# Performance work log

Hardware: AMD Instinct MI355X
Metric: run time of the kernel (lower is better)

Reference implementation:

```python
import jax, jax.numpy as jnp
import numpy as np

B, CIN, H, W = 8, 128, 64, 64
COUT, KH, KW = 128, 3, 3
STRIDE = (1, 1)
PAD = (1, 1)
DIL = (1, 1)
GROUPS = 1
OFFSET_GROUPS = 1

def _out_size(i, k, s, p, d):
    return (i + 2 * p - d * (k - 1) - 1) // s + 1

HO = _out_size(H, KH, STRIDE[0], PAD[0], DIL[0])
WO = _out_size(W, KW, STRIDE[1], PAD[1], DIL[1])


def setup_inputs() -> dict:
    key = jax.random.key(0)
    k1, k2, k3, k4 = jax.random.split(key, 4)
    x = jax.random.normal(k1, (B, CIN, H, W), jnp.float32)
    offset = jax.random.normal(k2, (B, 2 * OFFSET_GROUPS * KH * KW, HO, WO), jnp.float32)
    fan_in = (CIN // GROUPS) * KH * KW
    bound = 1.0 / np.sqrt(fan_in)
    weight = jax.random.uniform(k3, (COUT, CIN // GROUPS, KH, KW), jnp.float32, -bound, bound)
    bias = jax.random.uniform(k4, (COUT,), jnp.float32, -bound, bound)
    return {"x": x, "offset": offset, "weight": weight, "bias": bias}


def _deform_conv2d(x, offset, weight, bias):
    Bn, Cin, Hi, Wi = x.shape
    K = KH * KW
    Goff, Gw = OFFSET_GROUPS, GROUPS
    Cpg = Cin // Goff

    # base sampling positions (before learned offsets)
    ys = jnp.arange(HO, dtype=jnp.float32) * STRIDE[0] - PAD[0]  # [HO]
    xs = jnp.arange(WO, dtype=jnp.float32) * STRIDE[1] - PAD[1]  # [WO]
    base_y = jnp.repeat(jnp.arange(KH, dtype=jnp.float32) * DIL[0], KW)  # [K]
    base_x = jnp.tile(jnp.arange(KW, dtype=jnp.float32) * DIL[1], KH)    # [K]

    # offsets: channel layout is 2*(g*K + k) + {0: dy, 1: dx}
    off = offset.reshape(Bn, Goff, K, 2, HO, WO)
    py = base_y[None, None, :, None, None] + ys[None, None, None, :, None] + off[:, :, :, 0]  # [B,Goff,K,HO,WO]
    px = base_x[None, None, :, None, None] + xs[None, None, None, None, :] + off[:, :, :, 1]

    y0 = jnp.floor(py)
    x0 = jnp.floor(px)
    ly = py - y0  # fractional weights
    lx = px - x0

    xg = x.reshape(Bn, Goff, Cpg, Hi * Wi)

    def gather_one(img, lin):  # img [Cpg, H*W], lin [K,HO,WO] -> [Cpg,K,HO,WO]
        return img[:, lin]

    gather = jax.vmap(jax.vmap(gather_one))  # over B and Goff

    def corner(yi, xi, w):
        # zero-padding semantics: out-of-bounds corner contributes 0
        mask = (yi >= 0) & (yi < Hi) & (xi >= 0) & (xi < Wi)
        iy = jnp.clip(yi, 0, Hi - 1).astype(jnp.int32)
        ix = jnp.clip(xi, 0, Wi - 1).astype(jnp.int32)
        lin = iy * Wi + ix  # [B,Goff,K,HO,WO]
        wm = (w * mask.astype(x.dtype))[:, :, None]  # broadcast over channel axis
        return gather(xg, lin) * wm  # [B,Goff,Cpg,K,HO,WO]

    val = (corner(y0, x0, (1 - ly) * (1 - lx))
           + corner(y0, x0 + 1, (1 - ly) * lx)
           + corner(y0 + 1, x0, ly * (1 - lx))
           + corner(y0 + 1, x0 + 1, ly * lx))  # [B,Goff,Cpg,K,HO,WO]

    # grouped conv accumulate
    val = val.reshape(Bn, Gw, Cin // Gw, K, HO, WO)
    wg = weight.reshape(Gw, COUT // Gw, Cin // Gw, K)
    out = jnp.einsum('bgckhw,gock->bgohw', val, wg).reshape(Bn, COUT, HO, WO)
    return out + bias[None, :, None, None]


def reference(x, offset, weight, bias):
    return _deform_conv2d(x, offset, weight, bias)
```

## Files before the change

kernel.cpp:

```cpp
#include <hip/hip_runtime.h>

typedef unsigned int   u32;
typedef unsigned short u16;
typedef short bf16x8 __attribute__((ext_vector_type(8)));
typedef float f32x4  __attribute__((ext_vector_type(4)));

#define CIN   128
#define COUT  128
#define Hh    64
#define Ww    64
#define Bb    8
#define KPOS  9
#define KDIM  (CIN*KPOS)
#define NKSTEP 36
#define XT_ELEMS (Bb*Hh*Ww*CIN)

__device__ __forceinline__ float bflo(u32 u){ return __uint_as_float(u << 16); }
__device__ __forceinline__ float bfhi(u32 u){ return __uint_as_float(u & 0xffff0000u); }

__device__ __forceinline__ u32 packbf(float a, float b){
    u32 ua = __float_as_uint(a);
    u32 ub = __float_as_uint(b);
    ua += 0x7fffu + ((ua >> 16) & 1u);
    ub += 0x7fffu + ((ub >> 16) & 1u);
    return (ua >> 16) | (ub & 0xffff0000u);
}
__device__ __forceinline__ u16 tobf(float a){
    u32 ua = __float_as_uint(a);
    ua += 0x7fffu + ((ua >> 16) & 1u);
    return (u16)(ua >> 16);
}

__global__ __launch_bounds__(256) void k_transpose(const float* __restrict__ x,
                                                   u16* __restrict__ xT){
    __shared__ float tile[32*33];
    int bi = blockIdx.x;
    int st = bi & 127, ct = (bi >> 7) & 3, b = bi >> 9;
    int sb = st * 32, cb = ct * 32;
    int tid = threadIdx.x;

    int i = tid >> 5, j = tid & 31;
    const float* xp = x + ((size_t)(b*CIN + cb) * 4096) + sb;
#pragma unroll
    for (int rr = 0; rr < 4; ++rr){
        int ci = i + rr*8;
        tile[ci*33 + j] = xp[(size_t)ci*4096 + j];
    }
    __syncthreads();

    int ii = tid >> 4, jj = tid & 15;
    u32* outp = (u32*)xT + ((size_t)b*4096 + sb)*64 + (cb >> 1) + jj;
#pragma unroll
    for (int rr = 0; rr < 2; ++rr){
        int sl = ii + rr*16;
        float v0 = tile[(2*jj  )*33 + sl];
        float v1 = tile[(2*jj+1)*33 + sl];
        outp[(size_t)sl*64] = packbf(v0, v1);
    }
}

__global__ __launch_bounds__(256) void k_wprep(const float* __restrict__ w,
                                               u16* __restrict__ Wt){
    int gid = blockIdx.x*256 + threadIdx.x;
    int jf   = gid & 7;
    int lane = (gid >> 3) & 63;
    int mt   = (gid >> 9) & 7;
    int kt   = gid >> 12;
    int m  = mt*16 + (lane & 15);
    int kk = (lane >> 4)*8 + jf;
    int ck = kt*32 + kk;
    int kpos = ck >> 7;
    int cin  = ck & 127;
    Wt[gid] = tobf(w[((size_t)m*128 + cin)*9 + kpos]);
}

__global__ __launch_bounds__(256, 2)
void k_main(const float* __restrict__ off, const float* __restrict__ bias,
            const u16* __restrict__ xT, const u16* __restrict__ Wt,
            float* __restrict__ out){
    __shared__ u32 Vsm[2][64*20];

    int tid = threadIdx.x;
    int bi  = blockIdx.x;
    int b   = bi & 7;
    int t   = bi >> 3;
    int s0  = t * 64;

    int p  = tid >> 2, qt = tid & 3;
    int ho = t;
    int wo = p;
    const u16* xb_base = xT + (size_t)b * (Hh*Ww*CIN);

    int lane = tid & 63, wave = tid >> 6;
    int wm = wave >> 1, wn = wave & 1;
    int quad = lane >> 4, l16 = lane & 15;

    f32x4 acc[4][2];
#pragma unroll
    for (int i = 0; i < 4; ++i)
#pragma unroll
        for (int j = 0; j < 2; ++j) acc[i][j] = {0.f, 0.f, 0.f, 0.f};

    int   aa[4];
    float wt[4];

    auto state = [&](int kpos){
        int kh = kpos / 3, kw = kpos - kh*3;
        size_t ob = ((size_t)(b*18 + 2*kpos))*4096 + (s0 + p);
        float dy = off[ob];
        float dx = off[ob + 4096];
        float py = (float)(ho + kh - 1) + dy;
        float px = (float)(wo + kw - 1) + dx;
        float y0f = floorf(py), x0f = floorf(px);
        float ly = py - y0f, lx = px - x0f;
        int y0 = (int)y0f, x0 = (int)x0f;
        int y1 = y0 + 1,  x1 = x0 + 1;
        float my0 = (y0 >= 0 && y0 < Hh) ? 1.f : 0.f;
        float my1 = (y1 >= 0 && y1 < Hh) ? 1.f : 0.f;
        float mx0 = (x0 >= 0 && x0 < Ww) ? 1.f : 0.f;
        float mx1 = (x1 >= 0 && x1 < Ww) ? 1.f : 0.f;
        float omly = 1.f - ly, omlx = 1.f - lx;
        wt[0] = omly*omlx*my0*mx0;
        wt[1] = omly*lx  *my0*mx1;
        wt[2] = ly  *omlx*my1*mx0;
        wt[3] = ly  *lx  *my1*mx1;
        int cy0 = min(max(y0,0),Hh-1), cy1 = min(max(y1,0),Hh-1);
        int cx0 = min(max(x0,0),Ww-1), cx1 = min(max(x1,0),Ww-1);
        aa[0] = (cy0*Ww + cx0)*CIN;
        aa[1] = (cy0*Ww + cx1)*CIN;
        aa[2] = (cy1*Ww + cx0)*CIN;
        aa[3] = (cy1*Ww + cx1)*CIN;
    };

    auto gather = [&](int ks, uint4 q[4]){
        int coff = ((ks & 3) << 5) + qt*8;
        const u16* xb = xb_base + coff;
#pragma unroll
        for (int c = 0; c < 4; ++c)
            q[c] = *(const uint4*)(xb + aa[c]);
    };

    auto loadA = [&](int ks, uint4 a[4]){
#pragma unroll
        for (int i = 0; i < 4; ++i)
            a[i] = *(const uint4*)(Wt + (size_t)(((ks*8 + wm*4 + i)*64 + lane))*8);
    };

    auto blend_store = [&](const uint4 q[4], int buf){
        u32 res[4];
#pragma unroll
        for (int d = 0; d < 4; ++d){
            float lo = 0.f, hi = 0.f;
#pragma unroll
            for (int c = 0; c < 4; ++c){
                u32 u = ((const u32*)&q[0])[c*4 + d];
                lo = fmaf(wt[c], bflo(u), lo);
                hi = fmaf(wt[c], bfhi(u), hi);
            }
            res[d] = packbf(lo, hi);
        }
        *(uint4*)&Vsm[buf][p*20 + qt*4] = *(uint4*)&res[0];
    };

    uint4 q[4], araw_cur[4], araw_nxt[4];
    state(0);
    gather(0, q);
    loadA(0, araw_cur);
    blend_store(q, 0);

    for (int ks = 0; ks < NKSTEP; ++ks){
        __syncthreads();
        int nxt = ks + 1;
        bool have_nxt = (nxt < NKSTEP);
        if (have_nxt){
            if ((nxt & 3) == 0) state(nxt >> 2);
            gather(nxt, q);
            loadA(nxt, araw_nxt);
        }

        uint4 braw[2];
#pragma unroll
        for (int j = 0; j < 2; ++j)
            braw[j] = *(const uint4*)&Vsm[ks & 1][((wn*2 + j)*16 + l16)*20 + quad*4];
#pragma unroll
        for (int i = 0; i < 4; ++i){
            bf16x8 av = __builtin_bit_cast(bf16x8, araw_cur[i]);
#pragma unroll
            for (int j = 0; j < 2; ++j){
                bf16x8 bv = __builtin_bit_cast(bf16x8, braw[j]);
                acc[i][j] = __builtin_amdgcn_mfma_f32_16x16x32_bf16(av, bv, acc[i][j], 0, 0, 0);
            }
        }

        if (have_nxt){
            blend_store(q, nxt & 1);
#pragma unroll
            for (int i = 0; i < 4; ++i) araw_cur[i] = araw_nxt[i];
        }
    }

#pragma unroll
    for (int i = 0; i < 4; ++i){
        int cout0 = (wm*4 + i)*16 + quad*4;
#pragma unroll
        for (int j = 0; j < 2; ++j){
            int pcol = (wn*2 + j)*16 + l16;
            size_t obase = ((size_t)(b*COUT + cout0))*4096 + (s0 + pcol);
#pragma unroll
            for (int r = 0; r < 4; ++r){
                out[obase + (size_t)r*4096] = acc[i][j][r] + bias[cout0 + r];
            }
        }
    }
}

extern "C" void kernel_launch(void* const* d_in, const int* in_sizes, int n_in,
                              void* d_out, int out_size, void* d_ws, size_t ws_size,
                              hipStream_t stream){
    const float* x    = (const float*)d_in[0];
    const float* off  = (const float*)d_in[1];
    const float* w    = (const float*)d_in[2];
    const float* bias = (const float*)d_in[3];
    float* out = (float*)d_out;

    u16* xT = (u16*)d_ws;
    u16* Wt = xT + XT_ELEMS;

    k_transpose<<<dim3(4096), dim3(256), 0, stream>>>(x, xT);
    k_wprep    <<<dim3(576),  dim3(256), 0, stream>>>(w, Wt);
    k_main     <<<dim3(512),  dim3(256), 0, stream>>>(off, bias, xT, Wt, out);
}
```

Before: 109.0 us.

## Halve main-kernel pixel tile, raise occupancy, and vectorize transpose with cheaper bf16 pack

The main kernel now processes 32 output pixels per block instead of 64, with 8 threads per pixel gathering 4 channels each. This doubles the grid, halves LDS and accumulators, and raises the launch-bounds occupancy target to 4 blocks. The transpose kernel is rewritten so each block handles a full 64-pixel row across all 128 channels, using float4 loads and 16-byte packed stores. The bf16 packing switches from round-to-nearest-even to a round-half-up add plus byte-permute. The smaller tile reduces per-wave MFMA reuse of the weight fragments, since each A load now feeds one MFMA instead of two.

```diff
diff --git a/kernel.cpp b/kernel.cpp
--- a/kernel.cpp
+++ b/kernel.cpp
@@ -4,26 +4,23 @@
 typedef unsigned short u16;
 typedef short bf16x8 __attribute__((ext_vector_type(8)));
 typedef float f32x4  __attribute__((ext_vector_type(4)));
+typedef float f32x2  __attribute__((ext_vector_type(2)));
 
 #define CIN   128
 #define COUT  128
 #define Hh    64
 #define Ww    64
 #define Bb    8
-#define KPOS  9
-#define KDIM  (CIN*KPOS)
 #define NKSTEP 36
 #define XT_ELEMS (Bb*Hh*Ww*CIN)
 
 __device__ __forceinline__ float bflo(u32 u){ return __uint_as_float(u << 16); }
 __device__ __forceinline__ float bfhi(u32 u){ return __uint_as_float(u & 0xffff0000u); }
 
-__device__ __forceinline__ u32 packbf(float a, float b){
-    u32 ua = __float_as_uint(a);
-    u32 ub = __float_as_uint(b);
-    ua += 0x7fffu + ((ua >> 16) & 1u);
-    ub += 0x7fffu + ((ub >> 16) & 1u);
-    return (ua >> 16) | (ub & 0xffff0000u);
+__device__ __forceinline__ u32 pack2(float a, float b){
+    u32 lo = __float_as_uint(a) + 0x8000u;
+    u32 hi = __float_as_uint(b) + 0x8000u;
+    return __builtin_amdgcn_perm(hi, lo, 0x07060302u);
 }
 __device__ __forceinline__ u16 tobf(float a){
     u32 ua = __float_as_uint(a);
@@ -33,29 +30,41 @@
 
 __global__ __launch_bounds__(256) void k_transpose(const float* __restrict__ x,
                                                    u16* __restrict__ xT){
-    __shared__ float tile[32*33];
+    __shared__ float lds[64*132];
     int bi = blockIdx.x;
-    int st = bi & 127, ct = (bi >> 7) & 3, b = bi >> 9;
-    int sb = st * 32, cb = ct * 32;
+    int hb = bi & 63, b = bi >> 6;
     int tid = threadIdx.x;
 
-    int i = tid >> 5, j = tid & 31;
-    const float* xp = x + ((size_t)(b*CIN + cb) * 4096) + sb;
-#pragma unroll
-    for (int rr = 0; rr < 4; ++rr){
-        int ci = i + rr*8;
-        tile[ci*33 + j] = xp[(size_t)ci*4096 + j];
+    {
+        int r = tid >> 1, cq = tid & 1;
+        const float* xp = x + ((size_t)(b*128 + r))*4096 + hb*64 + cq*32;
+        float4 v[8];
+#pragma unroll
+        for (int k = 0; k < 8; ++k) v[k] = *(const float4*)(xp + k*4);
+        float* dst = lds + (cq*32)*132 + r;
+#pragma unroll
+        for (int k = 0; k < 8; ++k){
+            dst[(k*4+0)*132] = v[k].x;
+            dst[(k*4+1)*132] = v[k].y;
+            dst[(k*4+2)*132] = v[k].z;
+            dst[(k*4+3)*132] = v[k].w;
+        }
     }
     __syncthreads();
-
-    int ii = tid >> 4, jj = tid & 15;
-    u32* outp = (u32*)xT + ((size_t)b*4096 + sb)*64 + (cb >> 1) + jj;
-#pragma unroll
-    for (int rr = 0; rr < 2; ++rr){
-        int sl = ii + rr*16;
-        float v0 = tile[(2*jj  )*33 + sl];
-        float v1 = tile[(2*jj+1)*33 + sl];
-        outp[(size_t)sl*64] = packbf(v0, v1);
+    {
+        int s = tid >> 2, kq = tid & 3;
+        const float* src = lds + s*132 + kq*32;
+        u32 r16[16];
+#pragma unroll
+        for (int k = 0; k < 8; ++k){
+            float4 v = *(const float4*)(src + k*4);
+            r16[k*2  ] = pack2(v.x, v.y);
+            r16[k*2+1] = pack2(v.z, v.w);
+        }
+        u32* dst = (u32*)xT + ((size_t)(b*4096 + hb*64 + s))*64 + kq*16;
+#pragma unroll
+        for (int k = 0; k < 4; ++k)
+            *(uint4*)(dst + k*4) = *(uint4*)&r16[k*4];
     }
 }
 
@@ -74,32 +83,30 @@
     Wt[gid] = tobf(w[((size_t)m*128 + cin)*9 + kpos]);
 }
 
-__global__ __launch_bounds__(256, 2)
+__global__ __launch_bounds__(256, 4)
 void k_main(const float* __restrict__ off, const float* __restrict__ bias,
             const u16* __restrict__ xT, const u16* __restrict__ Wt,
             float* __restrict__ out){
-    __shared__ u32 Vsm[2][64*20];
+    __shared__ u32 Vsm[2][32*20];
 
     int tid = threadIdx.x;
     int bi  = blockIdx.x;
     int b   = bi & 7;
     int t   = bi >> 3;
-    int s0  = t * 64;
-
-    int p  = tid >> 2, qt = tid & 3;
-    int ho = t;
-    int wo = p;
-    const u16* xb_base = xT + (size_t)b * (Hh*Ww*CIN);
+    int s0  = t * 32;
+    int ho  = s0 >> 6, wo0 = s0 & 63;
+
+    int p = tid >> 3, o = tid & 7;
+    int wo = wo0 + p;
+    const u16* xb = xT + (size_t)b * (Hh*Ww*CIN);
 
     int lane = tid & 63, wave = tid >> 6;
     int wm = wave >> 1, wn = wave & 1;
     int quad = lane >> 4, l16 = lane & 15;
 
-    f32x4 acc[4][2];
-#pragma unroll
-    for (int i = 0; i < 4; ++i)
-#pragma unroll
-        for (int j = 0; j < 2; ++j) acc[i][j] = {0.f, 0.f, 0.f, 0.f};
+    f32x4 acc[4];
+#pragma unroll
+    for (int i = 0; i < 4; ++i) acc[i] = {0.f, 0.f, 0.f, 0.f};
 
     int   aa[4];
     float wt[4];
@@ -119,11 +126,11 @@
         float my1 = (y1 >= 0 && y1 < Hh) ? 1.f : 0.f;
         float mx0 = (x0 >= 0 && x0 < Ww) ? 1.f : 0.f;
         float mx1 = (x1 >= 0 && x1 < Ww) ? 1.f : 0.f;
-        float omly = 1.f - ly, omlx = 1.f - lx;
-        wt[0] = omly*omlx*my0*mx0;
-        wt[1] = omly*lx  *my0*mx1;
-        wt[2] = ly  *omlx*my1*mx0;
-        wt[3] = ly  *lx  *my1*mx1;
+        float oy = 1.f - ly, ox = 1.f - lx;
+        wt[0] = oy*ox*my0*mx0;
+        wt[1] = oy*lx*my0*mx1;
+        wt[2] = ly*ox*my1*mx0;
+        wt[3] = ly*lx*my1*mx1;
         int cy0 = min(max(y0,0),Hh-1), cy1 = min(max(y1,0),Hh-1);
         int cx0 = min(max(x0,0),Ww-1), cx1 = min(max(x1,0),Ww-1);
         aa[0] = (cy0*Ww + cx0)*CIN;
@@ -132,37 +139,40 @@
         aa[3] = (cy1*Ww + cx1)*CIN;
     };
 
-    auto gather = [&](int ks, uint4 q[4]){
-        int coff = ((ks & 3) << 5) + qt*8;
-        const u16* xb = xb_base + coff;
+    auto gather = [&](int ks, uint2 q[4]){
+        int coff = ((ks & 3) << 5) + o*4;
+        const u16* xc = xb + coff;
 #pragma unroll
         for (int c = 0; c < 4; ++c)
-            q[c] = *(const uint4*)(xb + aa[c]);
+            q[c] = *(const uint2*)(xc + aa[c]);
     };
 
     auto loadA = [&](int ks, uint4 a[4]){
+        const u16* wp = Wt + (size_t)((ks*8 + wm*4)*64 + lane)*8;
 #pragma unroll
         for (int i = 0; i < 4; ++i)
-            a[i] = *(const uint4*)(Wt + (size_t)(((ks*8 + wm*4 + i)*64 + lane))*8);
-    };
-
-    auto blend_store = [&](const uint4 q[4], int buf){
-        u32 res[4];
-#pragma unroll
-        for (int d = 0; d < 4; ++d){
-            float lo = 0.f, hi = 0.f;
+            a[i] = *(const uint4*)(wp + (size_t)i*64*8);
+    };
+
+    auto blend_store = [&](const uint2 q[4], int buf){
+        u32 r2[2];
+#pragma unroll
+        for (int d = 0; d < 2; ++d){
+            f32x2 s = {0.f, 0.f};
 #pragma unroll
             for (int c = 0; c < 4; ++c){
-                u32 u = ((const u32*)&q[0])[c*4 + d];
-                lo = fmaf(wt[c], bflo(u), lo);
-                hi = fmaf(wt[c], bfhi(u), hi);
+                u32 u = ((const u32*)q)[c*2 + d];
+                f32x2 v  = { bflo(u), bfhi(u) };
+                f32x2 w2 = { wt[c], wt[c] };
+                s += w2 * v;
             }
-            res[d] = packbf(lo, hi);
-        }
-        *(uint4*)&Vsm[buf][p*20 + qt*4] = *(uint4*)&res[0];
-    };
-
-    uint4 q[4], araw_cur[4], araw_nxt[4];
+            r2[d] = pack2(s.x, s.y);
+        }
+        *(uint2*)&Vsm[buf][p*20 + o*2] = *(uint2*)&r2[0];
+    };
+
+    uint2 q[4];
+    uint4 araw_cur[4], araw_nxt[4];
     state(0);
     gather(0, q);
     loadA(0, araw_cur);
@@ -178,18 +188,12 @@
             loadA(nxt, araw_nxt);
         }
 
-        uint4 braw[2];
-#pragma unroll
-        for (int j = 0; j < 2; ++j)
-            braw[j] = *(const uint4*)&Vsm[ks & 1][((wn*2 + j)*16 + l16)*20 + quad*4];
+        uint4 braw = *(const uint4*)&Vsm[ks & 1][(wn*16 + l16)*20 + quad*4];
+        bf16x8 bv = __builtin_bit_cast(bf16x8, braw);
 #pragma unroll
         for (int i = 0; i < 4; ++i){
             bf16x8 av = __builtin_bit_cast(bf16x8, araw_cur[i]);
-#pragma unroll
-            for (int j = 0; j < 2; ++j){
-                bf16x8 bv = __builtin_bit_cast(bf16x8, braw[j]);
-                acc[i][j] = __builtin_amdgcn_mfma_f32_16x16x32_bf16(av, bv, acc[i][j], 0, 0, 0);
-            }
+            acc[i] = __builtin_amdgcn_mfma_f32_16x16x32_bf16(av, bv, acc[i], 0, 0, 0);
         }
 
         if (have_nxt){
@@ -199,18 +203,14 @@
         }
     }
 
+    int pcol = wn*16 + l16;
 #pragma unroll
     for (int i = 0; i < 4; ++i){
         int cout0 = (wm*4 + i)*16 + quad*4;
-#pragma unroll
-        for (int j = 0; j < 2; ++j){
-            int pcol = (wn*2 + j)*16 + l16;
-            size_t obase = ((size_t)(b*COUT + cout0))*4096 + (s0 + pcol);
-#pragma unroll
-            for (int r = 0; r < 4; ++r){
-                out[obase + (size_t)r*4096] = acc[i][j][r] + bias[cout0 + r];
-            }
-        }
+        size_t obase = ((size_t)(b*COUT + cout0))*4096 + (s0 + pcol);
+#pragma unroll
+        for (int r = 0; r < 4; ++r)
+            out[obase + (size_t)r*4096] = acc[i][r] + bias[cout0 + r];
     }
 }
 
@@ -226,7 +226,7 @@
     u16* xT = (u16*)d_ws;
     u16* Wt = xT + XT_ELEMS;
 
-    k_transpose<<<dim3(4096), dim3(256), 0, stream>>>(x, xT);
+    k_transpose<<<dim3(512),  dim3(256), 0, stream>>>(x, xT);
     k_wprep    <<<dim3(576),  dim3(256), 0, stream>>>(w, Wt);
-    k_main     <<<dim3(512),  dim3(256), 0, stream>>>(off, bias, xT, Wt, out);
-}
+    k_main     <<<dim3(1024), dim3(256), 0, stream>>>(off, bias, xT, Wt, out);
+}
```

Measured after the change: 119.7 us. 1.1x slower.
